# Optimization experiments

Hardware: AMD Instinct MI355X
Metric: run time of the kernel (lower is better)

The kernel has to match this reference:

```python
import jax, jax.numpy as jnp
import numpy as np

D_MODEL = 1024
H = 16
D_K = 64
D_V = 64
D_HALF = D_MODEL // 2  # after_forget == after_summary dims


def setup_inputs() -> dict:
    key = jax.random.key(0)
    ks = jax.random.split(key, 16)
    B, NQ, NK = 2, 2048, 2048
    inp = {
        "queries": jax.random.normal(ks[0], (B, NQ, D_MODEL), jnp.float32),
        "keys": jax.random.normal(ks[1], (B, NK, D_MODEL), jnp.float32),
        "values": jax.random.normal(ks[2], (B, NK, D_MODEL), jnp.float32),
        "attn_mask": jax.random.randint(ks[3], (B, H, NQ, NK), 0, 2).astype(bool),
        "attn_weights": jax.random.uniform(ks[4], (B, H, NQ, NK), jnp.float32),
        # forget-gate linears (torch Linear: y = x @ W.T + b)
        "Wk_f": jax.random.normal(ks[5], (D_HALF, D_MODEL), jnp.float32) * (1.0 / np.sqrt(D_MODEL)),
        "bk_f": jnp.zeros((D_HALF,), jnp.float32),
        "kf_bias": jax.random.normal(ks[6], (1, 1, D_HALF), jnp.float32) * (1.0 / D_HALF),
        "Wv_f": jax.random.normal(ks[7], (D_HALF, D_MODEL), jnp.float32) * (1.0 / np.sqrt(D_MODEL)),
        "bv_f": jnp.zeros((D_HALF,), jnp.float32),
        "vf_bias": jax.random.normal(ks[8], (1, 1, D_HALF), jnp.float32) * (1.0 / D_HALF),
        # summary units
        "k_sum": jax.random.normal(ks[9], (1, 1, D_HALF), jnp.float32) * (1.0 / D_HALF),
        "v_sum": jax.random.normal(ks[10], (1, 1, D_HALF), jnp.float32) * (1.0 / D_HALF),
        # output projection
        "Wo": jax.random.normal(ks[11], (D_MODEL, H * D_V), jnp.float32) * (1.0 / np.sqrt(H * D_V)),
        "bo": jnp.zeros((D_MODEL,), jnp.float32),
    }
    return inp


def reference(queries, keys, values, attn_mask, attn_weights,
              Wk_f, bk_f, kf_bias, Wv_f, bv_f, vf_bias,
              k_sum, v_sum, Wo, bo):
    B, Nq, _ = queries.shape
    Nk = keys.shape[1]
    # forget-gated halves + broadcast summary halves -> full d_model width
    fk = jax.nn.sigmoid(keys @ Wk_f.T + bk_f + kf_bias)        # [B,Nk,D/2]
    fv = jax.nn.sigmoid(values @ Wv_f.T + bv_f + vf_bias)      # [B,Nk,D/2]
    uk = jnp.concatenate([fk, jnp.broadcast_to(k_sum, (B, Nk, D_HALF))], axis=-1)
    uv = jnp.concatenate([fv, jnp.broadcast_to(v_sum, (B, Nk, D_HALF))], axis=-1)
    q = queries.reshape(B, Nq, H, D_K)
    k = uk.reshape(B, Nk, H, D_K)
    v = uv.reshape(B, Nk, H, D_V)
    scores = jnp.einsum("bqhd,bkhd->bhqk", q, k) / np.sqrt(D_K).astype(np.float32)
    scores = scores * attn_weights
    scores = jnp.where(attn_mask, -jnp.inf, scores)
    probs = jax.nn.softmax(scores, axis=-1)                    # [B,H,Nq,Nk]
    out = jnp.einsum("bhqk,bkhd->bqhd", probs, v).reshape(B, Nq, H * D_V)
    return out @ Wo.T + bo
```

## Files before the change

### kernel.cpp

```cpp
#include <hip/hip_runtime.h>

typedef __attribute__((ext_vector_type(8))) short short8;
typedef __attribute__((ext_vector_type(4))) float f32x4;

__device__ __forceinline__ unsigned short f2bf(float f) {
    unsigned u = __float_as_uint(f);
    u += 0x7fffu + ((u >> 16) & 1u);
    return (unsigned short)(u >> 16);
}

__global__ __launch_bounds__(256) void k_compute_c(const float* __restrict__ Wo,
        const float* __restrict__ bo, const float* __restrict__ vsum, float* __restrict__ c) {
    int w = threadIdx.x >> 6, lane = threadIdx.x & 63;
    int j = blockIdx.x * 4 + w;
    const float* row = Wo + (size_t)j * 1024 + 512;
    float acc = 0.0f;
    #pragma unroll
    for (int i = 0; i < 8; ++i) acc = fmaf(row[lane + 64*i], vsum[lane + 64*i], acc);
    #pragma unroll
    for (int off = 32; off; off >>= 1) acc += __shfl_xor(acc, off);
    if (lane == 0) c[j] = acc + bo[j];
}

__global__ __launch_bounds__(256) void k_convq(const float* __restrict__ q, unsigned short* __restrict__ Qh) {
    int t = blockIdx.x * 256 + threadIdx.x;
    int e = t * 4;
    int c = e & 511;
    int bn = e >> 9;
    float4 v = *reinterpret_cast<const float4*>(q + (size_t)bn * 1024 + c);
    int h = c >> 6, d = c & 63;
    int b = bn >> 11, n = bn & 2047;
    ushort4 o;
    o.x = f2bf(v.x * 0.125f); o.y = f2bf(v.y * 0.125f);
    o.z = f2bf(v.z * 0.125f); o.w = f2bf(v.w * 0.125f);
    *reinterpret_cast<ushort4*>(Qh + (((size_t)(b*8+h) * 2048 + n) * 64 + d)) = o;
}

__global__ __launch_bounds__(256) void k_gate(const float* __restrict__ X, const float* __restrict__ W,
        const float* __restrict__ b1, const float* __restrict__ b2,
        unsigned short* __restrict__ out) {
    __shared__ __align__(16) unsigned short Xs[64*88];
    __shared__ __align__(16) unsigned short Wsh[64*88];
    int t = threadIdx.x;
    int mbase = blockIdx.x * 64, nbase = blockIdx.y * 64;
    int w = t >> 6, lane = t & 63, l = lane & 15, quad = lane >> 4;
    int srow = t >> 2, sk = (t & 3) * 16;
    f32x4 acc[4] = {};
    for (int kk = 0; kk < 1024; kk += 64) {
        const float4* xs = reinterpret_cast<const float4*>(X + (size_t)(mbase+srow)*1024 + kk + sk);
        const float4* wsp = reinterpret_cast<const float4*>(W + (size_t)(nbase+srow)*1024 + kk + sk);
        #pragma unroll
        for (int i = 0; i < 4; ++i) {
            float4 xv = xs[i], wv = wsp[i];
            ushort4 xo, wo;
            xo.x=f2bf(xv.x); xo.y=f2bf(xv.y); xo.z=f2bf(xv.z); xo.w=f2bf(xv.w);
            wo.x=f2bf(wv.x); wo.y=f2bf(wv.y); wo.z=f2bf(wv.z); wo.w=f2bf(wv.w);
            *reinterpret_cast<ushort4*>(&Xs[srow*88 + sk + i*4]) = xo;
            *reinterpret_cast<ushort4*>(&Wsh[srow*88 + sk + i*4]) = wo;
        }
        __syncthreads();
        short8 a0 = *reinterpret_cast<const short8*>(&Xs[(w*16+l)*88 + quad*8]);
        short8 a1 = *reinterpret_cast<const short8*>(&Xs[(w*16+l)*88 + 32 + quad*8]);
        #pragma unroll
        for (int nt = 0; nt < 4; ++nt) {
            short8 bq0 = *reinterpret_cast<const short8*>(&Wsh[(l+16*nt)*88 + quad*8]);
            short8 bq1 = *reinterpret_cast<const short8*>(&Wsh[(l+16*nt)*88 + 32 + quad*8]);
            acc[nt] = __builtin_amdgcn_mfma_f32_16x16x32_bf16(a0, bq0, acc[nt], 0, 0, 0);
            acc[nt] = __builtin_amdgcn_mfma_f32_16x16x32_bf16(a1, bq1, acc[nt], 0, 0, 0);
        }
        __syncthreads();
    }
    #pragma unroll
    for (int nt = 0; nt < 4; ++nt) {
        int col = nbase + l + 16*nt;
        float bias = b1[col] + b2[col];
        #pragma unroll
        for (int reg = 0; reg < 4; ++reg) {
            int m = mbase + w*16 + quad*4 + reg;
            float x = acc[nt][reg] + bias;
            float g = 1.0f / (1.0f + __expf(-x));
            int b = m >> 11, n = m & 2047;
            int h = col >> 6, d = col & 63;
            out[(((size_t)(b*8+h)*2048 + n)*64 + d)] = f2bf(g);
        }
    }
}

__global__ __launch_bounds__(256) void k_vtrans(const unsigned short* __restrict__ Vn,
        unsigned short* __restrict__ Vt) {
    __shared__ __align__(16) unsigned short T[64*72];
    int bh = blockIdx.y;
    int n0 = blockIdx.x * 64;
    int t = threadIdx.x;
    int r = t >> 2, c = (t & 3) * 16;
    const unsigned short* src = Vn + ((size_t)bh*2048 + n0 + r)*64 + c;
    short8 v0 = *reinterpret_cast<const short8*>(src);
    short8 v1 = *reinterpret_cast<const short8*>(src + 8);
    *reinterpret_cast<short8*>(&T[r*72 + c]) = v0;
    *reinterpret_cast<short8*>(&T[r*72 + c + 8]) = v1;
    __syncthreads();
    int d = t >> 2, oc = (t & 3) * 16;
    unsigned short tmp[16];
    #pragma unroll
    for (int j = 0; j < 16; ++j) tmp[j] = T[(oc + j)*72 + d];
    unsigned short* dst = Vt + ((size_t)bh*64 + d)*2048 + n0 + oc;
    *reinterpret_cast<short8*>(dst) = *reinterpret_cast<short8*>(&tmp[0]);
    *reinterpret_cast<short8*>(dst + 8) = *reinterpret_cast<short8*>(&tmp[8]);
}

#define NEGBIG -1e30f
__global__ __launch_bounds__(256) void k_attn(const unsigned short* __restrict__ Qh,
        const unsigned short* __restrict__ Kh, const unsigned short* __restrict__ Vt,
        const float* __restrict__ attw, const int* __restrict__ mask,
        unsigned short* __restrict__ O) {
    __shared__ __align__(16) float Fs[2][64*68];
    __shared__ __align__(16) unsigned short Ps[4*16*88];
    int bx = blockIdx.x;
    int qt = bx & 31, h = (bx >> 5) & 7, b = bx >> 8;
    int t = threadIdx.x, w = t >> 6, lane = t & 63, l = lane & 15, quad = lane >> 4;
    int qbase = qt * 64;
    int bh = b*8 + h;
    const unsigned short* qp = Qh + ((size_t)bh*2048 + qbase + w*16 + l)*64 + quad*8;
    short8 qf0 = *reinterpret_cast<const short8*>(qp);
    short8 qf1 = *reinterpret_cast<const short8*>(qp + 32);
    float m_r[4], l_r[4];
    f32x4 oacc[4] = {};
    #pragma unroll
    for (int r = 0; r < 4; ++r) { m_r[r] = NEGBIG; l_r[r] = 0.0f; }
    unsigned short* Pw = &Ps[w * 16*88];

    int srow = t >> 2, scol = (t & 3) * 16;
    const float* awp = attw + ((size_t)((b*16 + h)*2048 + qbase + srow))*2048 + scol;
    const int*   mkp = mask + ((size_t)((b*16 + h)*2048 + qbase + srow))*2048 + scol;
    float4 aw[4];
    int4   mkv[4];

    #pragma unroll
    for (int i = 0; i < 4; ++i) {
        aw[i]  = *reinterpret_cast<const float4*>(awp + i*4);
        mkv[i] = *reinterpret_cast<const int4*>(mkp + i*4);
    }
    {
        float* dst = &Fs[0][srow*68 + scol];
        #pragma unroll
        for (int i = 0; i < 4; ++i) {
            float4 fv;
            fv.x = mkv[i].x ? NEGBIG : aw[i].x;
            fv.y = mkv[i].y ? NEGBIG : aw[i].y;
            fv.z = mkv[i].z ? NEGBIG : aw[i].z;
            fv.w = mkv[i].w ? NEGBIG : aw[i].w;
            *reinterpret_cast<float4*>(dst + i*4) = fv;
        }
    }
    __syncthreads();

    for (int kt = 0; kt < 32; ++kt) {
        int kbase = kt * 64;
        if (kt < 31) {
            const float* a2 = awp + (kt+1)*64;
            const int*   m2 = mkp + (kt+1)*64;
            #pragma unroll
            for (int i = 0; i < 4; ++i) {
                aw[i]  = *reinterpret_cast<const float4*>(a2 + i*4);
                mkv[i] = *reinterpret_cast<const int4*>(m2 + i*4);
            }
        }
        f32x4 s[4] = {};
        #pragma unroll
        for (int nt = 0; nt < 4; ++nt) {
            const unsigned short* kp = Kh + ((size_t)bh*2048 + kbase + l + 16*nt)*64 + quad*8;
            short8 k0 = *reinterpret_cast<const short8*>(kp);
            short8 k1 = *reinterpret_cast<const short8*>(kp + 32);
            s[nt] = __builtin_amdgcn_mfma_f32_16x16x32_bf16(qf0, k0, s[nt], 0, 0, 0);
            s[nt] = __builtin_amdgcn_mfma_f32_16x16x32_bf16(qf1, k1, s[nt], 0, 0, 0);
        }
        const float* fbuf = &Fs[kt & 1][0];
        float sv[4][4];
        #pragma unroll
        for (int reg = 0; reg < 4; ++reg) {
            int rowoff = (w*16 + quad*4 + reg) * 68 + l;
            #pragma unroll
            for (int nt = 0; nt < 4; ++nt) {
                float f = fbuf[rowoff + 16*nt];
                sv[nt][reg] = (f < -5e29f) ? NEGBIG : s[nt][reg] * f;
            }
        }
        float alpha[4];
        #pragma unroll
        for (int reg = 0; reg < 4; ++reg) {
            float rm = fmaxf(fmaxf(sv[0][reg], sv[1][reg]), fmaxf(sv[2][reg], sv[3][reg]));
            rm = fmaxf(rm, __shfl_xor(rm, 1));
            rm = fmaxf(rm, __shfl_xor(rm, 2));
            rm = fmaxf(rm, __shfl_xor(rm, 4));
            rm = fmaxf(rm, __shfl_xor(rm, 8));
            float mnew = fmaxf(m_r[reg], rm);
            alpha[reg] = __expf(m_r[reg] - mnew);
            m_r[reg] = mnew;
            float rs = 0.0f;
            #pragma unroll
            for (int nt = 0; nt < 4; ++nt) {
                float p = __expf(sv[nt][reg] - mnew);
                sv[nt][reg] = p;
                rs += p;
            }
            rs += __shfl_xor(rs, 1);
            rs += __shfl_xor(rs, 2);
            rs += __shfl_xor(rs, 4);
            rs += __shfl_xor(rs, 8);
            l_r[reg] = l_r[reg] * alpha[reg] + rs;
        }
        #pragma unroll
        for (int dt = 0; dt < 4; ++dt)
            #pragma unroll
            for (int reg = 0; reg < 4; ++reg)
                oacc[dt][reg] *= alpha[reg];
        #pragma unroll
        for (int reg = 0; reg < 4; ++reg)
            #pragma unroll
            for (int nt = 0; nt < 4; ++nt)
                Pw[(quad*4+reg)*88 + l + 16*nt] = f2bf(sv[nt][reg]);
        __builtin_amdgcn_s_waitcnt(0xC07F);
        short8 pf0 = *reinterpret_cast<const short8*>(&Pw[l*88 + quad*8]);
        short8 pf1 = *reinterpret_cast<const short8*>(&Pw[l*88 + 32 + quad*8]);
        #pragma unroll
        for (int dt = 0; dt < 4; ++dt) {
            const unsigned short* vp = Vt + ((size_t)bh*64 + l + 16*dt)*2048 + kbase + quad*8;
            short8 v0 = *reinterpret_cast<const short8*>(vp);
            short8 v1 = *reinterpret_cast<const short8*>(vp + 32);
            oacc[dt] = __builtin_amdgcn_mfma_f32_16x16x32_bf16(pf0, v0, oacc[dt], 0, 0, 0);
            oacc[dt] = __builtin_amdgcn_mfma_f32_16x16x32_bf16(pf1, v1, oacc[dt], 0, 0, 0);
        }
        if (kt < 31) {
            float* dst = &Fs[(kt+1) & 1][srow*68 + scol];
            #pragma unroll
            for (int i = 0; i < 4; ++i) {
                float4 fv;
                fv.x = mkv[i].x ? NEGBIG : aw[i].x;
                fv.y = mkv[i].y ? NEGBIG : aw[i].y;
                fv.z = mkv[i].z ? NEGBIG : aw[i].z;
                fv.w = mkv[i].w ? NEGBIG : aw[i].w;
                *reinterpret_cast<float4*>(dst + i*4) = fv;
            }
        }
        __syncthreads();
    }
    #pragma unroll
    for (int reg = 0; reg < 4; ++reg) {
        float inv = 1.0f / l_r[reg];
        int qr = qbase + w*16 + quad*4 + reg;
        #pragma unroll
        for (int dt = 0; dt < 4; ++dt) {
            int col = h*64 + l + 16*dt;
            O[((size_t)b*2048 + qr)*512 + col] = f2bf(oacc[dt][reg] * inv);
        }
    }
}

__global__ __launch_bounds__(256) void k_proj(const unsigned short* __restrict__ O,
        const float* __restrict__ Wo, const float* __restrict__ c, float* __restrict__ out) {
    __shared__ __align__(16) unsigned short Wsh[64*88];
    int t = threadIdx.x;
    int mb = blockIdx.x * 64, nb = blockIdx.y * 64;
    int w = t >> 6, lane = t & 63, l = lane & 15, quad = lane >> 4;
    int srow = t >> 2, sk = (t & 3) * 16;
    f32x4 acc[4] = {};
    for (int kb = 0; kb < 512; kb += 64) {
        const float4* wp = reinterpret_cast<const float4*>(Wo + (size_t)(nb+srow)*1024 + kb + sk);
        #pragma unroll
        for (int i = 0; i < 4; ++i) {
            float4 wv = wp[i];
            ushort4 wo2;
            wo2.x=f2bf(wv.x); wo2.y=f2bf(wv.y); wo2.z=f2bf(wv.z); wo2.w=f2bf(wv.w);
            *reinterpret_cast<ushort4*>(&Wsh[srow*88 + sk + i*4]) = wo2;
        }
        __syncthreads();
        const unsigned short* op = O + (size_t)(mb + w*16 + l)*512 + kb + quad*8;
        short8 a0 = *reinterpret_cast<const short8*>(op);
        short8 a1 = *reinterpret_cast<const short8*>(op + 32);
        #pragma unroll
        for (int nt = 0; nt < 4; ++nt) {
            short8 b0 = *reinterpret_cast<const short8*>(&Wsh[(l+16*nt)*88 + quad*8]);
            short8 b1 = *reinterpret_cast<const short8*>(&Wsh[(l+16*nt)*88 + 32 + quad*8]);
            acc[nt] = __builtin_amdgcn_mfma_f32_16x16x32_bf16(a0, b0, acc[nt], 0, 0, 0);
            acc[nt] = __builtin_amdgcn_mfma_f32_16x16x32_bf16(a1, b1, acc[nt], 0, 0, 0);
        }
        __syncthreads();
    }
    #pragma unroll
    for (int nt = 0; nt < 4; ++nt) {
        int coln = nb + l + 16*nt;
        float cv = c[coln];
        #pragma unroll
        for (int reg = 0; reg < 4; ++reg) {
            int row = mb + w*16 + quad*4 + reg;
            out[(size_t)row*1024 + coln] = acc[nt][reg] + cv;
        }
    }
}

extern "C" void kernel_launch(void* const* d_in, const int* in_sizes, int n_in,
                              void* d_out, int out_size, void* d_ws, size_t ws_size,
                              hipStream_t stream) {
    const float* queries = (const float*)d_in[0];
    const float* keys    = (const float*)d_in[1];
    const float* values  = (const float*)d_in[2];
    const int*   mask    = (const int*)d_in[3];
    const float* attw    = (const float*)d_in[4];
    const float* Wk_f    = (const float*)d_in[5];
    const float* bk_f    = (const float*)d_in[6];
    const float* kf_bias = (const float*)d_in[7];
    const float* Wv_f    = (const float*)d_in[8];
    const float* bv_f    = (const float*)d_in[9];
    const float* vf_bias = (const float*)d_in[10];
    const float* v_sum   = (const float*)d_in[12];
    const float* Wo      = (const float*)d_in[13];
    const float* bo      = (const float*)d_in[14];
    float* out = (float*)d_out;

    char* ws = (char*)d_ws;
    float* cvec = (float*)ws;
    unsigned short* Qh = (unsigned short*)(ws + 4096);
    unsigned short* Kh = Qh + (size_t)2*8*2048*64;
    unsigned short* Vt = Kh + (size_t)2*8*2048*64;
    unsigned short* Vn = Vt + (size_t)2*8*2048*64;
    unsigned short* Ob = Vn;

    hipLaunchKernelGGL(k_compute_c, dim3(256), dim3(256), 0, stream, Wo, bo, v_sum, cvec);
    hipLaunchKernelGGL(k_convq, dim3(2048), dim3(256), 0, stream, queries, Qh);
    hipLaunchKernelGGL(k_gate, dim3(64, 8), dim3(256), 0, stream, keys, Wk_f, bk_f, kf_bias, Kh);
    hipLaunchKernelGGL(k_gate, dim3(64, 8), dim3(256), 0, stream, values, Wv_f, bv_f, vf_bias, Vn);
    hipLaunchKernelGGL(k_vtrans, dim3(32, 16), dim3(256), 0, stream, Vn, Vt);
    hipLaunchKernelGGL(k_attn, dim3(512), dim3(256), 0, stream, Qh, Kh, Vt, attw, mask, Ob);
    hipLaunchKernelGGL(k_proj, dim3(64, 16), dim3(256), 0, stream, Ob, Wo, cvec, out);
}
```

Measured before the change: 1.108 ms.

## Split attention key range across wave pairs and load mask/weights directly into registers

The attention kernel now gives each block 32 query rows and splits the key dimension in half across pairs of waves, merging the two partial softmax states through shared memory at the end (split-K flash attention). The grid doubles to 1024 blocks for more parallelism. Attention weights and mask are now loaded straight into registers with scalar strided loads and double-buffered prefetch, which removes the shared-memory staging buffer and the per-iteration block barrier. The trade-off is uncoalesced 4-byte global loads in place of float4 loads, more register pressure, and an extra merge step.

```diff
diff --git a/kernel.cpp b/kernel.cpp
--- a/kernel.cpp
+++ b/kernel.cpp
@@ -113,14 +113,16 @@
         const unsigned short* __restrict__ Kh, const unsigned short* __restrict__ Vt,
         const float* __restrict__ attw, const int* __restrict__ mask,
         unsigned short* __restrict__ O) {
-    __shared__ __align__(16) float Fs[2][64*68];
     __shared__ __align__(16) unsigned short Ps[4*16*88];
+    __shared__ __align__(16) float Og[2][16*64];
+    __shared__ float Ml[2][2][16];
     int bx = blockIdx.x;
-    int qt = bx & 31, h = (bx >> 5) & 7, b = bx >> 8;
+    int qt = bx & 63, h = (bx >> 6) & 7, b = bx >> 9;
     int t = threadIdx.x, w = t >> 6, lane = t & 63, l = lane & 15, quad = lane >> 4;
-    int qbase = qt * 64;
+    int qgrp = w >> 1, kh = w & 1;
+    int qbase = qt * 32 + qgrp * 16;
     int bh = b*8 + h;
-    const unsigned short* qp = Qh + ((size_t)bh*2048 + qbase + w*16 + l)*64 + quad*8;
+    const unsigned short* qp = Qh + ((size_t)bh*2048 + qbase + l)*64 + quad*8;
     short8 qf0 = *reinterpret_cast<const short8*>(qp);
     short8 qf1 = *reinterpret_cast<const short8*>(qp + 32);
     float m_r[4], l_r[4];
@@ -128,42 +130,31 @@
     #pragma unroll
     for (int r = 0; r < 4; ++r) { m_r[r] = NEGBIG; l_r[r] = 0.0f; }
     unsigned short* Pw = &Ps[w * 16*88];
-
-    int srow = t >> 2, scol = (t & 3) * 16;
-    const float* awp = attw + ((size_t)((b*16 + h)*2048 + qbase + srow))*2048 + scol;
-    const int*   mkp = mask + ((size_t)((b*16 + h)*2048 + qbase + srow))*2048 + scol;
-    float4 aw[4];
-    int4   mkv[4];
-
-    #pragma unroll
-    for (int i = 0; i < 4; ++i) {
-        aw[i]  = *reinterpret_cast<const float4*>(awp + i*4);
-        mkv[i] = *reinterpret_cast<const int4*>(mkp + i*4);
-    }
-    {
-        float* dst = &Fs[0][srow*68 + scol];
-        #pragma unroll
-        for (int i = 0; i < 4; ++i) {
-            float4 fv;
-            fv.x = mkv[i].x ? NEGBIG : aw[i].x;
-            fv.y = mkv[i].y ? NEGBIG : aw[i].y;
-            fv.z = mkv[i].z ? NEGBIG : aw[i].z;
-            fv.w = mkv[i].w ? NEGBIG : aw[i].w;
-            *reinterpret_cast<float4*>(dst + i*4) = fv;
-        }
-    }
-    __syncthreads();
-
-    for (int kt = 0; kt < 32; ++kt) {
-        int kbase = kt * 64;
-        if (kt < 31) {
-            const float* a2 = awp + (kt+1)*64;
-            const int*   m2 = mkp + (kt+1)*64;
-            #pragma unroll
-            for (int i = 0; i < 4; ++i) {
-                aw[i]  = *reinterpret_cast<const float4*>(a2 + i*4);
-                mkv[i] = *reinterpret_cast<const int4*>(m2 + i*4);
-            }
+    const size_t fbase = ((size_t)((b*16 + h)*2048 + qbase + quad*4))*2048 + l;
+    const int khbase = kh * 1024;
+
+    float awA[16], awB[16];
+    int   mkA[16], mkB[16];
+
+    #pragma unroll
+    for (int reg = 0; reg < 4; ++reg)
+        #pragma unroll
+        for (int nt = 0; nt < 4; ++nt) {
+            size_t off = fbase + (size_t)reg*2048 + khbase + 16*nt;
+            awA[reg*4+nt] = attw[off];
+            mkA[reg*4+nt] = mask[off];
+        }
+
+    auto body = [&](int kbase, float* awc, int* mkc, float* awn, int* mkn, bool pref) {
+        if (pref) {
+            #pragma unroll
+            for (int reg = 0; reg < 4; ++reg)
+                #pragma unroll
+                for (int nt = 0; nt < 4; ++nt) {
+                    size_t off = fbase + (size_t)reg*2048 + (kbase + 64) + 16*nt;
+                    awn[reg*4+nt] = attw[off];
+                    mkn[reg*4+nt] = mask[off];
+                }
         }
         f32x4 s[4] = {};
         #pragma unroll
@@ -174,17 +165,12 @@
             s[nt] = __builtin_amdgcn_mfma_f32_16x16x32_bf16(qf0, k0, s[nt], 0, 0, 0);
             s[nt] = __builtin_amdgcn_mfma_f32_16x16x32_bf16(qf1, k1, s[nt], 0, 0, 0);
         }
-        const float* fbuf = &Fs[kt & 1][0];
         float sv[4][4];
         #pragma unroll
-        for (int reg = 0; reg < 4; ++reg) {
-            int rowoff = (w*16 + quad*4 + reg) * 68 + l;
-            #pragma unroll
-            for (int nt = 0; nt < 4; ++nt) {
-                float f = fbuf[rowoff + 16*nt];
-                sv[nt][reg] = (f < -5e29f) ? NEGBIG : s[nt][reg] * f;
-            }
-        }
+        for (int reg = 0; reg < 4; ++reg)
+            #pragma unroll
+            for (int nt = 0; nt < 4; ++nt)
+                sv[nt][reg] = mkc[reg*4+nt] ? NEGBIG : s[nt][reg] * awc[reg*4+nt];
         float alpha[4];
         #pragma unroll
         for (int reg = 0; reg < 4; ++reg) {
@@ -230,28 +216,45 @@
             oacc[dt] = __builtin_amdgcn_mfma_f32_16x16x32_bf16(pf0, v0, oacc[dt], 0, 0, 0);
             oacc[dt] = __builtin_amdgcn_mfma_f32_16x16x32_bf16(pf1, v1, oacc[dt], 0, 0, 0);
         }
-        if (kt < 31) {
-            float* dst = &Fs[(kt+1) & 1][srow*68 + scol];
-            #pragma unroll
-            for (int i = 0; i < 4; ++i) {
-                float4 fv;
-                fv.x = mkv[i].x ? NEGBIG : aw[i].x;
-                fv.y = mkv[i].y ? NEGBIG : aw[i].y;
-                fv.z = mkv[i].z ? NEGBIG : aw[i].z;
-                fv.w = mkv[i].w ? NEGBIG : aw[i].w;
-                *reinterpret_cast<float4*>(dst + i*4) = fv;
+    };
+
+    for (int i = 0; i < 8; ++i) {
+        body(khbase + (2*i)*64,   awA, mkA, awB, mkB, true);
+        body(khbase + (2*i+1)*64, awB, mkB, awA, mkA, i < 7);
+    }
+
+    if (kh == 1) {
+        #pragma unroll
+        for (int dt = 0; dt < 4; ++dt)
+            #pragma unroll
+            for (int reg = 0; reg < 4; ++reg)
+                Og[qgrp][(quad*4+reg)*64 + l + 16*dt] = oacc[dt][reg];
+        if (l == 0) {
+            #pragma unroll
+            for (int reg = 0; reg < 4; ++reg) {
+                Ml[qgrp][0][quad*4+reg] = m_r[reg];
+                Ml[qgrp][1][quad*4+reg] = l_r[reg];
             }
         }
-        __syncthreads();
-    }
-    #pragma unroll
-    for (int reg = 0; reg < 4; ++reg) {
-        float inv = 1.0f / l_r[reg];
-        int qr = qbase + w*16 + quad*4 + reg;
-        #pragma unroll
-        for (int dt = 0; dt < 4; ++dt) {
-            int col = h*64 + l + 16*dt;
-            O[((size_t)b*2048 + qr)*512 + col] = f2bf(oacc[dt][reg] * inv);
+    }
+    __syncthreads();
+    if (kh == 0) {
+        #pragma unroll
+        for (int reg = 0; reg < 4; ++reg) {
+            int row = quad*4 + reg;
+            float m1 = Ml[qgrp][0][row];
+            float l1 = Ml[qgrp][1][row];
+            float mstar = fmaxf(m_r[reg], m1);
+            float a0 = __expf(m_r[reg] - mstar);
+            float a1 = __expf(m1 - mstar);
+            float inv = 1.0f / (l_r[reg]*a0 + l1*a1);
+            int qr = qbase + row;
+            #pragma unroll
+            for (int dt = 0; dt < 4; ++dt) {
+                float v1 = Og[qgrp][row*64 + l + 16*dt];
+                float val = (oacc[dt][reg]*a0 + v1*a1) * inv;
+                O[((size_t)b*2048 + qr)*512 + h*64 + l + 16*dt] = f2bf(val);
+            }
         }
     }
 }
@@ -330,6 +333,6 @@
     hipLaunchKernelGGL(k_gate, dim3(64, 8), dim3(256), 0, stream, keys, Wk_f, bk_f, kf_bias, Kh);
     hipLaunchKernelGGL(k_gate, dim3(64, 8), dim3(256), 0, stream, values, Wv_f, bv_f, vf_bias, Vn);
     hipLaunchKernelGGL(k_vtrans, dim3(32, 16), dim3(256), 0, stream, Vn, Vt);
-    hipLaunchKernelGGL(k_attn, dim3(512), dim3(256), 0, stream, Qh, Kh, Vt, attw, mask, Ob);
+    hipLaunchKernelGGL(k_attn, dim3(1024), dim3(256), 0, stream, Qh, Kh, Vt, attw, mask, Ob);
     hipLaunchKernelGGL(k_proj, dim3(64, 16), dim3(256), 0, stream, Ob, Wo, cvec, out);
 }
```

Result: faster. 1.075 ms (-2.9%).
